# Performance work log

Measured on AMD Instinct MI355X. Metric: run time of the kernel, lower is better.

## Reference

```python
import jax, jax.numpy as jnp
import numpy as np

N_GRID, N_IO = 99872, 128   # height*width, n_inputs+n_outputs
N = N_GRID + N_IO           # 100000 nodes
E = 1600000                 # edges before self-loops
HID, WID = 128, 128         # hidden_dim, network_width (heads=1)


def _ln(h, g, b, eps=1e-5):
    mu = jnp.mean(h, axis=-1, keepdims=True)
    v = jnp.mean((h - mu) ** 2, axis=-1, keepdims=True)
    return (h - mu) * jax.lax.rsqrt(v + eps) * g + b


def setup_inputs() -> dict:
    ks = jax.random.split(jax.random.key(0), 32)
    r = lambda i, sh, s=0.05: jax.random.normal(ks[i], sh, jnp.float32) * s
    return {
        "x": jax.random.normal(ks[0], (N, HID + 2), jnp.float32),
        "edge_index": jax.random.randint(ks[1], (2, E), 0, N),
        "initial": r(2, (N_IO, HID)),
        "Wf1": r(3, (HID + 2, WID)), "bf1": r(4, (WID,)),
        "Wf2": r(5, (WID, HID + 2)), "bf2": r(6, (HID + 2,)),
        "Wu1": r(7, (HID + 2, WID)), "bu1": r(8, (WID,)),
        "Wu2": r(9, (WID, HID)), "bu2": r(10, (HID,)),
        "Wc1": r(11, (HID + 2, WID)), "bc1": r(12, (WID,)),
        "Wc2": r(13, (WID, WID)), "bc2": r(14, (WID,)),
        "Wc3": r(15, (WID, WID)), "bc3": r(16, (WID,)),
        "Wc4": r(17, (WID, WID)), "bc4": r(18, (WID,)),
        "Wco": r(19, (WID, HID)), "bco": r(20, (HID,)),
        "g3": jnp.ones((WID,), jnp.float32), "bn3": jnp.zeros((WID,), jnp.float32),
        "g6": jnp.ones((WID,), jnp.float32), "bn6": jnp.zeros((WID,), jnp.float32),
        "g7": jnp.ones((WID,), jnp.float32), "bn7": jnp.zeros((WID,), jnp.float32),
    }


def _step(x, initial, Wf1, bf1, Wf2, bf2, Wu1, bu1, Wu2, bu2,
          Wc1, bc1, Wc2, bc2, Wc3, bc3, Wc4, bc4, Wco, bco,
          g3, bn3, g6, bn6, g7, bn7, edge_index):
    # GCNConv: add self-loops, symmetric deg^-1/2 normalization, max-aggregation.
    loops = jnp.arange(N)
    row = jnp.concatenate([edge_index[0], loops])  # source
    col = jnp.concatenate([edge_index[1], loops])  # target
    deg = jax.ops.segment_sum(jnp.ones(row.shape[0], x.dtype), col, num_segments=N)
    dinv = jnp.where(deg > 0, jax.lax.rsqrt(deg), 0.0)
    norm = dinv[row] * dinv[col]  # [E+N]

    def gcn(h, W, b):
        m = (h @ W)[row] * norm[:, None]                      # gather + scale
        return jax.ops.segment_max(m, col, num_segments=N) + b  # scatter-max

    # forget gate, mixing toward the (padded) initial state
    f = jax.nn.sigmoid(jax.nn.sigmoid(x @ Wf1 + bf1) @ Wf2 + bf2)  # [N, HID+2]
    init_pad = jnp.concatenate([jnp.zeros((N_GRID, HID), x.dtype), initial], axis=0)
    init_pad = jnp.concatenate([init_pad, jnp.zeros((N, 2), x.dtype)], axis=1)
    x = x * f + (1.0 - f) * init_pad

    # update gate
    u = jax.nn.sigmoid(jax.nn.sigmoid(x @ Wu1 + bu1) @ Wu2 + bu2)  # [N, HID]

    h = jax.nn.relu(_ln(gcn(x, Wc1, bc1), g3, bn3))
    h = _ln(gcn(h, Wc2, bc2), g3, bn3)   # layer_norm3 reused, as in source
    h = _ln(gcn(h, Wc3, bc3), g6, bn6)
    h = _ln(gcn(h, Wc4, bc4), g7, bn7)
    h = gcn(h, Wco, bco)                 # [N, HID]
    return x[:, :-2] + h * u


def reference(x, edge_index, initial, Wf1, bf1, Wf2, bf2, Wu1, bu1, Wu2, bu2,
              Wc1, bc1, Wc2, bc2, Wc3, bc3, Wc4, bc4, Wco, bco,
              g3, bn3, g6, bn6, g7, bn7):
    return _step(x, initial, Wf1, bf1, Wf2, bf2, Wu1, bu1, Wu2, bu2,
                 Wc1, bc1, Wc2, bc2, Wc3, bc3, Wc4, bc4, Wco, bco,
                 g3, bn3, g6, bn6, g7, bn7, edge_index)
```

## Files before the change

kernel.cpp:

```cpp
#include <hip/hip_runtime.h>
#include <cstdint>

#define HID 128
#define HC  130
#define NIO 128
#define DENSW 64
#define SUBB 8
#define BCAP_S 128

typedef _Float16 f16;
typedef _Float16 f16x2 __attribute__((ext_vector_type(2)));
typedef _Float16 f16x4 __attribute__((ext_vector_type(4)));
typedef _Float16 f16x8 __attribute__((ext_vector_type(8)));
typedef float    f32x4 __attribute__((ext_vector_type(4)));

__device__ __forceinline__ float sigm(float z) {
  return 1.0f / (1.0f + __expf(-z));
}

__device__ __forceinline__ int xcc_id() {
  int x;
  asm volatile("s_getreg_b32 %0, hwreg(HW_REG_XCC_ID)" : "=s"(x));
  return x & 7;
}

__device__ __forceinline__ f16x8 max8(f16x8 a, f16x8 b) {
  union P { f16x8 h; f16x2 p[4]; } A, B, O;
  A.h = a; B.h = b;
  #pragma unroll
  for (int i = 0; i < 4; ++i)
    asm("v_pk_max_f16 %0, %1, %2" : "=v"(O.p[i]) : "v"(A.p[i]), "v"(B.p[i]));
  return O.h;
}

struct WDesc { const float* src; f16* dst; int K, NC, Kpad, NCpad; };
struct WAll { WDesc m[9]; };

__global__ __launch_bounds__(256) void prep_kernel(
    const float* __restrict__ x, f16* __restrict__ x16, f16* __restrict__ xg,
    int n, WAll wa, int* __restrict__ bcnt, int nzero, int gX) {
  const int bb = blockIdx.x;
  const int t = threadIdx.x;
  if (bb < gX) {
    int idx = bb * 256 + t;
    if (idx >= n * 20) return;
    int r = idx / 20, g = idx - r * 20;
    int c0 = g * 8;
    f16x8 o;
    #pragma unroll
    for (int j = 0; j < 8; ++j) {
      int c = c0 + j;
      o[j] = (f16)((c < HC) ? x[(size_t)r * HC + c] : 0.0f);
    }
    *(f16x8*)&x16[(size_t)r * 160 + c0] = o;
    if (c0 >= 136) {
      f16x8 z = (f16x8){0,0,0,0,0,0,0,0};
      *(f16x8*)&xg[(size_t)r * 160 + c0] = z;
    } else if (c0 == 128) {
      #pragma unroll
      for (int c = 130; c < 136; ++c) xg[(size_t)r * 160 + c] = (f16)0.0f;
    }
  } else if (bb < gX + 90) {
    const int wb = bb - gX;
    const WDesc d = wa.m[wb / 10];
    const int KST = d.Kpad >> 5;
    const int total = (d.NCpad >> 4) * KST * 64;
    int idx = (wb % 10) * 256 + t;
    if (idx >= total) return;
    int nt  = idx / (KST * 64);
    int rem = idx - nt * (KST * 64);
    int ks  = rem >> 6;
    int l   = rem & 63;
    int nn  = nt * 16 + (l & 15);
    int k0  = ks * 32 + (l >> 4) * 8;
    f16x8 o;
    #pragma unroll
    for (int j = 0; j < 8; ++j) {
      int k = k0 + j;
      float v = (k < d.K && nn < d.NC) ? d.src[(size_t)k * d.NC + nn] : 0.0f;
      o[j] = (f16)v;
    }
    *((f16x8*)d.dst + idx) = o;
  } else {
    int i = (bb - gX - 90) * 256 + t;
    if (i < nzero) bcnt[i] = 0;
  }
}

__global__ void binscatter_kernel(const int* __restrict__ row, const int* __restrict__ col,
    int* __restrict__ bcnt, unsigned* __restrict__ bucket, int e, int nb) {
  const int g0 = xcc_id() * SUBB + ((blockIdx.x >> 3) & (SUBB - 1));
  int i = blockIdx.x * blockDim.x + threadIdx.x;
  if (i >= e) return;
  int c = col[i], r = row[i];
  int b = c >> 7;
  int cur = atomicAdd(&bcnt[g0 * nb + b], 1);
  if (cur < BCAP_S)
    bucket[((size_t)g0 * nb + b) * BCAP_S + cur] = ((unsigned)r << 7) | (unsigned)(c & 127);
}

__global__ __launch_bounds__(256) void build_kernel(const int* __restrict__ bcnt,
    const unsigned* __restrict__ bucket, int* __restrict__ ncnt,
    int* __restrict__ dense, float* __restrict__ dinv, int n, int nb) {
  __shared__ int lcnt[128];
  const int b = blockIdx.x;
  const int t = threadIdx.x;
  if (t < 128) lcnt[t] = 0;
  __syncthreads();
  const int wv = t >> 6, ln = t & 63;
  #pragma unroll 1
  for (int g = wv * 16; g < wv * 16 + 16; ++g) {
    const int cntg = min(bcnt[g * nb + b], BCAP_S);
    const unsigned* __restrict__ src = bucket + ((size_t)g * nb + b) * BCAP_S;
    for (int idx = ln; idx < cntg; idx += 64) {
      unsigned ev = src[idx];
      int cl = (int)(ev & 127u);
      int r  = (int)(ev >> 7);
      int s = atomicAdd(&lcnt[cl], 1);
      if (s < DENSW) dense[(size_t)((b << 7) + cl) * DENSW + s] = r;
    }
  }
  __syncthreads();
  if (t < 128) {
    int c = (b << 7) + t;
    if (c < n) {
      int cc = min(lcnt[t], DENSW);
      ncnt[c] = cc;
      dinv[c] = rsqrtf((float)(cc + 1));
    }
  }
}

template<int KPAD, int RS, int NCPAD, int NC, int MODE, int MROWS>
__global__ __launch_bounds__(256, 4) void mm_mfma(
    const f16* __restrict__ X, const f16* __restrict__ Wt,
    const float* __restrict__ bias, f16* __restrict__ Y,
    const float* __restrict__ dinv, const f16* __restrict__ xor16,
    const float* __restrict__ initial, int n, int ngrid)
{
  static_assert(MODE != 1 || MROWS == 128, "MODE1 only at 128 rows");
  constexpr int KST = KPAD / 32;
  constexpr int NT  = NCPAD / 16;
  constexpr int MT  = MROWS / 64;
  constexpr int RPW = MROWS / 4;
  constexpr int YRS = (MODE == 1) ? 160 : 128;
  constexpr int PSTR = (NCPAD == 128) ? 132 : 148;
  constexpr int LDSH = (NCPAD * KPAD > MROWS * PSTR) ? NCPAD * KPAD : MROWS * PSTR;
  __shared__ __align__(16) f16 Bs[LDSH];

  const int t = threadIdx.x;
  const int wid  = t >> 6;
  const int l    = t & 63;
  const int m15  = l & 15;
  const int quad = l >> 4;
  const int rw   = blockIdx.x * MROWS + wid * RPW;

  constexpr int BSW = NCPAD * KPAD / 8;
  #pragma unroll
  for (int i = 0; i < (BSW + 255) / 256; ++i) {
    int idx = t + i * 256;
    if (BSW % 256 == 0 || idx < BSW)
      ((f16x8*)Bs)[idx] = ((const f16x8*)Wt)[idx];
  }

  const f16* Xr0 = X + (size_t)(rw + m15) * RS;
  const f16* Xr1 = X + (size_t)(rw + 16 + m15) * RS;
  f16x8 a0r[KST], a1r[KST];
  #pragma unroll
  for (int ks = 0; ks < KST; ++ks) {
    const int off = ks * 32 + quad * 8;
    a0r[ks] = *(const f16x8*)(Xr0 + off);
    if constexpr (MT == 2) a1r[ks] = *(const f16x8*)(Xr1 + off);
  }

  constexpr int TPR = 256 / MROWS;
  constexpr int CSP = 128 / TPR;
  const int r  = t / TPR;
  const int cp = t % TPR;
  const int gr = blockIdx.x * MROWS + r;
  float dv = 0.0f;
  if constexpr (MODE == 2) dv = (gr < n) ? dinv[gr] : 0.0f;

  f16x8 xo[CSP / 8];
  f16x2 xo2;
  if constexpr (MODE == 1) {
    const f16* xp = xor16 + (size_t)gr * 160;
    #pragma unroll
    for (int c8 = 0; c8 < CSP / 8; ++c8)
      xo[c8] = *(const f16x8*)(xp + cp * CSP + c8 * 8);
    xo2 = *(const f16x2*)(xp + 128);
  }

  __syncthreads();

  f32x4 acc[MT][NT];
  #pragma unroll
  for (int mt = 0; mt < MT; ++mt)
    #pragma unroll
    for (int nt = 0; nt < NT; ++nt)
      acc[mt][nt] = (f32x4){0.f, 0.f, 0.f, 0.f};

  #pragma unroll
  for (int ks = 0; ks < KST; ++ks) {
    #pragma unroll
    for (int nt = 0; nt < NT; ++nt) {
      f16x8 b = *((const f16x8*)Bs + (nt * KST + ks) * 64 + l);
      acc[0][nt] = __builtin_amdgcn_mfma_f32_16x16x32_f16(a0r[ks], b, acc[0][nt], 0, 0, 0);
      if constexpr (MT == 2)
        acc[1][nt] = __builtin_amdgcn_mfma_f32_16x16x32_f16(a1r[ks], b, acc[1][nt], 0, 0, 0);
    }
  }

  __syncthreads();

  #pragma unroll
  for (int mt = 0; mt < MT; ++mt) {
    #pragma unroll
    for (int reg = 0; reg < 4; ++reg) {
      const int rl = wid * RPW + mt * 16 + quad * 4 + reg;
      #pragma unroll
      for (int nt = 0; nt < NT; ++nt)
        Bs[rl * PSTR + nt * 16 + m15] = (f16)acc[mt][nt][reg];
    }
  }
  __syncthreads();

  if (gr < n) {
    if constexpr (MODE == 0 || MODE == 2) {
      #pragma unroll
      for (int c8 = 0; c8 < CSP / 8; ++c8) {
        const int c0 = cp * CSP + c8 * 8;
        f16x8 v = *(const f16x8*)&Bs[r * PSTR + c0];
        f16x8 o;
        #pragma unroll
        for (int j = 0; j < 8; ++j) {
          float a = (float)v[j];
          if constexpr (MODE == 0) o[j] = (f16)sigm(a + bias[c0 + j]);
          else                     o[j] = (f16)(a * dv);
        }
        *(f16x8*)&Y[(size_t)gr * YRS + c0] = o;
      }
    } else {
      const bool hasInit = (gr >= ngrid);
      #pragma unroll
      for (int c8 = 0; c8 < CSP / 8; ++c8) {
        const int c0 = cp * CSP + c8 * 8;
        f16x8 v = *(const f16x8*)&Bs[r * PSTR + c0];
        f16x8 o;
        #pragma unroll
        for (int j = 0; j < 8; ++j) {
          const int col = c0 + j;
          float fv = sigm((float)v[j] + bias[col]);
          float xov = (float)xo[c8][j];
          float ip = hasInit ? initial[(size_t)(gr - ngrid) * 128 + col] : 0.0f;
          o[j] = (f16)(xov * fv + (1.0f - fv) * ip);
        }
        *(f16x8*)&Y[(size_t)gr * YRS + c0] = o;
      }
      if (cp == 1) {
        #pragma unroll
        for (int k = 0; k < 2; ++k) {
          const int col = 128 + k;
          float fv = sigm((float)Bs[r * PSTR + col] + bias[col]);
          Y[(size_t)gr * YRS + col] = (f16)((float)xo2[k] * fv);
        }
      }
    }
  }
}

template<int K1PAD, int RS1, int NC2PAD, int NC2, int MODE2>
__global__ __launch_bounds__(256, 2) void mm_fused(
    const f16* __restrict__ X, const f16* __restrict__ W1t, const f16* __restrict__ W2t,
    const float* __restrict__ b1, const float* __restrict__ b2, f16* __restrict__ Y,
    const f16* __restrict__ xor16, const float* __restrict__ initial, int n, int ngrid)
{
  constexpr int KST1 = K1PAD / 32;
  constexpr int NT1  = 8;
  constexpr int KST2 = 4;
  constexpr int NT2  = NC2PAD / 16;
  constexpr int PSTR1 = 132;
  constexpr int PSTR2 = (NC2PAD == 128) ? 132 : 148;
  constexpr int YRS  = (MODE2 == 1) ? 160 : 128;
  constexpr int W2U  = NC2PAD * 128;
  constexpr int SC_A = K1PAD * 128;
  constexpr int SC_B = 128 * PSTR2;
  constexpr int SCU  = (SC_A > SC_B) ? SC_A : SC_B;
  __shared__ __align__(16) f16 L[W2U + SCU];
  f16* Bs2 = L;
  f16* SC  = L + W2U;

  const int t = threadIdx.x;
  const int wid  = t >> 6;
  const int l    = t & 63;
  const int m15  = l & 15;
  const int quad = l >> 4;
  const int rw   = blockIdx.x * 128 + wid * 32;

  constexpr int W1W = K1PAD * 128 / 8;
  constexpr int W2W = NC2PAD * 128 / 8;
  for (int i = t; i < W1W; i += 256) ((f16x8*)SC)[i]  = ((const f16x8*)W1t)[i];
  for (int i = t; i < W2W; i += 256) ((f16x8*)Bs2)[i] = ((const f16x8*)W2t)[i];

  const f16* Xr0 = X + (size_t)(rw + m15) * RS1;
  const f16* Xr1 = X + (size_t)(rw + 16 + m15) * RS1;
  f16x8 a0r[KST1], a1r[KST1];
  #pragma unroll
  for (int ks = 0; ks < KST1; ++ks) {
    const int off = ks * 32 + quad * 8;
    a0r[ks] = *(const f16x8*)(Xr0 + off);
    a1r[ks] = *(const f16x8*)(Xr1 + off);
  }

  f16x8 xo[8];
  f16x2 xo2;
  if constexpr (MODE2 == 1) {
    const f16* xp = xor16 + (size_t)(blockIdx.x * 128 + (t >> 1)) * 160;
    #pragma unroll
    for (int c8 = 0; c8 < 8; ++c8)
      xo[c8] = *(const f16x8*)(xp + (t & 1) * 64 + c8 * 8);
    xo2 = *(const f16x2*)(xp + 128);
  }

  float b1r[NT1];
  #pragma unroll
  for (int nt = 0; nt < NT1; ++nt) b1r[nt] = b1[nt * 16 + m15];

  __syncthreads();

  f32x4 acc1[2][NT1];
  #pragma unroll
  for (int mt = 0; mt < 2; ++mt)
    #pragma unroll
    for (int nt = 0; nt < NT1; ++nt)
      acc1[mt][nt] = (f32x4){0.f, 0.f, 0.f, 0.f};

  #pragma unroll
  for (int ks = 0; ks < KST1; ++ks) {
    #pragma unroll
    for (int nt = 0; nt < NT1; ++nt) {
      f16x8 b = *((const f16x8*)SC + (nt * KST1 + ks) * 64 + l);
      acc1[0][nt] = __builtin_amdgcn_mfma_f32_16x16x32_f16(a0r[ks], b, acc1[0][nt], 0, 0, 0);
      acc1[1][nt] = __builtin_amdgcn_mfma_f32_16x16x32_f16(a1r[ks], b, acc1[1][nt], 0, 0, 0);
    }
  }

  __syncthreads();

  #pragma unroll
  for (int mt = 0; mt < 2; ++mt) {
    #pragma unroll
    for (int reg = 0; reg < 4; ++reg) {
      const int rl = wid * 32 + mt * 16 + quad * 4 + reg;
      #pragma unroll
      for (int nt = 0; nt < NT1; ++nt)
        SC[rl * PSTR1 + nt * 16 + m15] = (f16)sigm(acc1[mt][nt][reg] + b1r[nt]);
    }
  }
  __syncthreads();

  f32x4 acc2[2][NT2];
  #pragma unroll
  for (int mt = 0; mt < 2; ++mt)
    #pragma unroll
    for (int nt = 0; nt < NT2; ++nt)
      acc2[mt][nt] = (f32x4){0.f, 0.f, 0.f, 0.f};

  const int rA0 = wid * 32 + m15;
  const int rA1 = rA0 + 16;
  union A8 { f16x8 v; f16x4 q[2]; };
  #pragma unroll
  for (int ks = 0; ks < KST2; ++ks) {
    const int k0 = ks * 32 + quad * 8;
    A8 a0, a1;
    a0.q[0] = *(const f16x4*)&SC[rA0 * PSTR1 + k0];
    a0.q[1] = *(const f16x4*)&SC[rA0 * PSTR1 + k0 + 4];
    a1.q[0] = *(const f16x4*)&SC[rA1 * PSTR1 + k0];
    a1.q[1] = *(const f16x4*)&SC[rA1 * PSTR1 + k0 + 4];
    #pragma unroll
    for (int nt = 0; nt < NT2; ++nt) {
      f16x8 b = *((const f16x8*)Bs2 + (nt * KST2 + ks) * 64 + l);
      acc2[0][nt] = __builtin_amdgcn_mfma_f32_16x16x32_f16(a0.v, b, acc2[0][nt], 0, 0, 0);
      acc2[1][nt] = __builtin_amdgcn_mfma_f32_16x16x32_f16(a1.v, b, acc2[1][nt], 0, 0, 0);
    }
  }
  __syncthreads();

  #pragma unroll
  for (int mt = 0; mt < 2; ++mt) {
    #pragma unroll
    for (int reg = 0; reg < 4; ++reg) {
      const int rl = wid * 32 + mt * 16 + quad * 4 + reg;
      #pragma unroll
      for (int nt = 0; nt < NT2; ++nt)
        SC[rl * PSTR2 + nt * 16 + m15] = (f16)acc2[mt][nt][reg];
    }
  }
  __syncthreads();

  const int r  = t >> 1;
  const int hf = t & 1;
  const int gr = blockIdx.x * 128 + r;
  if (gr < n) {
    if constexpr (MODE2 == 0) {
      #pragma unroll
      for (int c8 = 0; c8 < 8; ++c8) {
        const int c0 = hf * 64 + c8 * 8;
        f16x8 v = *(const f16x8*)&SC[r * PSTR2 + c0];
        f16x8 o;
        #pragma unroll
        for (int j = 0; j < 8; ++j)
          o[j] = (f16)sigm((float)v[j] + b2[c0 + j]);
        *(f16x8*)&Y[(size_t)gr * YRS + c0] = o;
      }
    } else {
      const bool hasInit = (gr >= ngrid);
      #pragma unroll
      for (int c8 = 0; c8 < 8; ++c8) {
        const int c0 = hf * 64 + c8 * 8;
        f16x8 v = *(const f16x8*)&SC[r * PSTR2 + c0];
        f16x8 o;
        #pragma unroll
        for (int j = 0; j < 8; ++j) {
          const int col = c0 + j;
          float fv = sigm((float)v[j] + b2[col]);
          float xov = (float)xo[c8][j];
          float ip = hasInit ? initial[(size_t)(gr - ngrid) * 128 + col] : 0.0f;
          o[j] = (f16)(xov * fv + (1.0f - fv) * ip);
        }
        *(f16x8*)&Y[(size_t)gr * YRS + c0] = o;
      }
      if (hf) {
        #pragma unroll
        for (int k = 0; k < 2; ++k) {
          const int col = 128 + k;
          float fv = sigm((float)SC[r * PSTR2 + col] + b2[col]);
          Y[(size_t)gr * YRS + col] = (f16)((float)xo2[k] * fv);
        }
      }
    }
  }
}

template<int MODE>
__global__ __launch_bounds__(256) void agg_kernel(
    const f16* __restrict__ G, const int* __restrict__ ncnt,
    const int* __restrict__ dense,
    const float* __restrict__ dinv, const float* __restrict__ bias,
    const float* __restrict__ gamma, const float* __restrict__ beta,
    const f16* __restrict__ xg, const f16* __restrict__ u,
    void* __restrict__ out, int n)
{
  const int wid = threadIdx.x >> 6, lane = threadIdx.x & 63;
  const int c = blockIdx.x * 4 + wid;
  if (c >= n) return;
  const int li = lane & 15, grp = lane >> 4;

  union F8 { f16x8 h; int4 i; };
  const int nc = min(ncnt[c], DENSW);
  int raw = 0;
  if (lane < 32) raw = dense[(size_t)c * DENSW + lane];
  if (nc > 32) {
    if (lane >= 32) raw = dense[(size_t)c * DENSW + lane];
  }
  const int myidx = (lane < nc) ? raw : c;

  F8 m; m.h = *(const f16x8*)(G + (size_t)c * 128 + li * 8);
  F8 m2; m2.h = m.h;
  F8 m3; m3.h = m.h;
  F8 m4; m4.h = m.h;
  const int B = (nc + 3) >> 2;
  int b = 0;
  for (; b + 3 < B; b += 4) {
    int r0 = __shfl(myidx, (b + 0) * 4 + grp, 64);
    int r1 = __shfl(myidx, (b + 1) * 4 + grp, 64);
    int r2 = __shfl(myidx, (b + 2) * 4 + grp, 64);
    int r3 = __shfl(myidx, (b + 3) * 4 + grp, 64);
    F8 v0; v0.h = *(const f16x8*)(G + (size_t)r0 * 128 + li * 8);
    F8 v1; v1.h = *(const f16x8*)(G + (size_t)r1 * 128 + li * 8);
    F8 v2; v2.h = *(const f16x8*)(G + (size_t)r2 * 128 + li * 8);
    F8 v3; v3.h = *(const f16x8*)(G + (size_t)r3 * 128 + li * 8);
    m.h  = max8(m.h,  v0.h);
    m2.h = max8(m2.h, v1.h);
    m3.h = max8(m3.h, v2.h);
    m4.h = max8(m4.h, v3.h);
  }
  for (; b < B; ++b) {
    int r0 = __shfl(myidx, b * 4 + grp, 64);
    F8 v; v.h = *(const f16x8*)(G + (size_t)r0 * 128 + li * 8);
    m.h = max8(m.h, v.h);
  }
  m.h = max8(max8(m.h, m2.h), max8(m3.h, m4.h));

  #pragma unroll
  for (int st = 16; st <= 32; st <<= 1) {
    F8 o;
    #pragma unroll
    for (int d = 0; d < 4; ++d) o.i[d] = __shfl_xor(m.i[d], st, 64);
    m.h = max8(m.h, o.h);
  }

  const float dc = dinv[c];
  float v[8];
  float s = 0.f, sq = 0.f;
  #pragma unroll
  for (int j = 0; j < 8; ++j) {
    v[j] = (float)m.h[j] * dc + bias[li * 8 + j];
    s += v[j]; sq += v[j] * v[j];
  }

  if constexpr (MODE == 2) {
    if (grp == 0) {
      f16x8 xv = *(const f16x8*)(xg + (size_t)c * 160 + li * 8);
      f16x8 uv = *(const f16x8*)(u  + (size_t)c * 128 + li * 8);
      float o[8];
      #pragma unroll
      for (int j = 0; j < 8; ++j) o[j] = (float)xv[j] + v[j] * (float)uv[j];
      float* op = (float*)out + (size_t)c * 128 + li * 8;
      *(float4*)op       = make_float4(o[0], o[1], o[2], o[3]);
      *(float4*)(op + 4) = make_float4(o[4], o[5], o[6], o[7]);
    }
  } else {
    #pragma unroll
    for (int st = 1; st <= 8; st <<= 1) {
      s  += __shfl_xor(s, st, 64);
      sq += __shfl_xor(sq, st, 64);
    }
    float mu  = s * (1.0f / 128.0f);
    float var = sq * (1.0f / 128.0f) - mu * mu;
    float rstd = rsqrtf(var + 1e-5f);
    if (grp == 0) {
      f16x8 ov;
      #pragma unroll
      for (int j = 0; j < 8; ++j) {
        float o = (v[j] - mu) * rstd * gamma[li * 8 + j] + beta[li * 8 + j];
        if constexpr (MODE == 0) o = fmaxf(o, 0.0f);
        ov[j] = (f16)o;
      }
      *(f16x8*)((f16*)out + (size_t)c * 128 + li * 8) = ov;
    }
  }
}

extern "C" void kernel_launch(void* const* d_in, const int* in_sizes, int n_in,
                              void* d_out, int out_size, void* d_ws, size_t ws_size,
                              hipStream_t stream) {
  (void)n_in; (void)out_size; (void)ws_size;
  const float* x       = (const float*)d_in[0];
  const int*   ei      = (const int*)d_in[1];
  const float* initial = (const float*)d_in[2];
  const float* Wf1 = (const float*)d_in[3];  const float* bf1 = (const float*)d_in[4];
  const float* Wf2 = (const float*)d_in[5];  const float* bf2 = (const float*)d_in[6];
  const float* Wu1 = (const float*)d_in[7];  const float* bu1 = (const float*)d_in[8];
  const float* Wu2 = (const float*)d_in[9];  const float* bu2 = (const float*)d_in[10];
  const float* Wc1 = (const float*)d_in[11]; const float* bc1 = (const float*)d_in[12];
  const float* Wc2 = (const float*)d_in[13]; const float* bc2 = (const float*)d_in[14];
  const float* Wc3 = (const float*)d_in[15]; const float* bc3 = (const float*)d_in[16];
  const float* Wc4 = (const float*)d_in[17]; const float* bc4 = (const float*)d_in[18];
  const float* Wco = (const float*)d_in[19]; const float* bco = (const float*)d_in[20];
  const float* g3  = (const float*)d_in[21]; const float* bn3 = (const float*)d_in[22];
  const float* g6  = (const float*)d_in[23]; const float* bn6 = (const float*)d_in[24];
  const float* g7  = (const float*)d_in[25]; const float* bn7 = (const float*)d_in[26];

  const int N  = in_sizes[0] / HC;
  const int E  = in_sizes[1] / 2;
  const int NG = N - NIO;
  const int NP = N + 128;
  const int NB = (N + 127) / 128;
  const int NSEG = 8 * SUBB;

  char* w = (char*)d_ws;
  auto carve = [&](size_t bytes) {
    char* p = w; w += (bytes + 255) & ~(size_t)255; return p;
  };
  int*      bcnt   = (int*)     carve((size_t)NB * NSEG * 4);
  unsigned* bucket = (unsigned*)carve((size_t)NB * NSEG * BCAP_S * 4);
  int*      ncnt   = (int*)     carve((size_t)N * 4);
  int*      dense  = (int*)     carve((size_t)N * DENSW * 4);
  float*    dinv   = (float*)   carve((size_t)N * 4);
  f16*      x16    = (f16*)     carve((size_t)NP * 160 * 2);
  f16*      xg     = (f16*)     carve((size_t)NP * 160 * 2);
  f16*      u      = (f16*)     carve((size_t)N  * 128 * 2);
  f16*      G      = (f16*)     carve((size_t)N  * 128 * 2);
  f16*      H      = (f16*)     carve((size_t)NP * 128 * 2);
  f16*      Wt_f1  = (f16*)     carve(160 * 128 * 2);
  f16*      Wt_f2  = (f16*)     carve(128 * 144 * 2);
  f16*      Wt_u1  = (f16*)     carve(160 * 128 * 2);
  f16*      Wt_u2  = (f16*)     carve(128 * 128 * 2);
  f16*      Wt_c1  = (f16*)     carve(160 * 128 * 2);
  f16*      Wt_c2  = (f16*)     carve(128 * 128 * 2);
  f16*      Wt_c3  = (f16*)     carve(128 * 128 * 2);
  f16*      Wt_c4  = (f16*)     carve(128 * 128 * 2);
  f16*      Wt_co  = (f16*)     carve(128 * 128 * 2);

  const int* erow = ei;
  const int* ecol = ei + E;

  const int gE  = (E + 255) / 256;
  const int gM  = (N + 127) / 128;
  const int gM64 = (N + 63) / 64;
  const int gA  = (N + 3) / 4;

  WAll wa;
  wa.m[0] = {Wf1, Wt_f1, HC,  HID, 160, 128};
  wa.m[1] = {Wf2, Wt_f2, HID, HC,  128, 144};
  wa.m[2] = {Wu1, Wt_u1, HC,  HID, 160, 128};
  wa.m[3] = {Wu2, Wt_u2, HID, HID, 128, 128};
  wa.m[4] = {Wc1, Wt_c1, HC,  HID, 160, 128};
  wa.m[5] = {Wc2, Wt_c2, HID, HID, 128, 128};
  wa.m[6] = {Wc3, Wt_c3, HID, HID, 128, 128};
  wa.m[7] = {Wc4, Wt_c4, HID, HID, 128, 128};
  wa.m[8] = {Wco, Wt_co, HID, HID, 128, 128};
  const int gX = (N * 20 + 255) / 256;
  const int gZ = (NB * NSEG + 255) / 256;
  prep_kernel<<<gX + 90 + gZ, 256, 0, stream>>>(x, x16, xg, N, wa, bcnt, NB * NSEG, gX);

  binscatter_kernel<<<gE, 256, 0, stream>>>(erow, ecol, bcnt, bucket, E, NB);
  build_kernel<<<NB, 256, 0, stream>>>(bcnt, bucket, ncnt, dense, dinv, N, NB);

  mm_fused<160, 160, 144, 130, 1><<<gM, 256, 0, stream>>>(
      x16, Wt_f1, Wt_f2, bf1, bf2, xg, x16, initial, N, NG);
  mm_fused<160, 160, 128, 128, 0><<<gM, 256, 0, stream>>>(
      xg, Wt_u1, Wt_u2, bu1, bu2, u, nullptr, nullptr, N, NG);

  mm_mfma<160, 160, 128, 128, 2, 64><<<gM64, 256, 0, stream>>>(xg, Wt_c1, nullptr, G, dinv, nullptr, nullptr, N, NG);
  agg_kernel<0><<<gA, 256, 0, stream>>>(G, ncnt, dense, dinv, bc1, g3, bn3, nullptr, nullptr, H, N);
  mm_mfma<128, 128, 128, 128, 2, 64><<<gM64, 256, 0, stream>>>(H, Wt_c2, nullptr, G, dinv, nullptr, nullptr, N, NG);
  agg_kernel<1><<<gA, 256, 0, stream>>>(G, ncnt, dense, dinv, bc2, g3, bn3, nullptr, nullptr, H, N);
  mm_mfma<128, 128, 128, 128, 2, 64><<<gM64, 256, 0, stream>>>(H, Wt_c3, nullptr, G, dinv, nullptr, nullptr, N, NG);
  agg_kernel<1><<<gA, 256, 0, stream>>>(G, ncnt, dense, dinv, bc3, g6, bn6, nullptr, nullptr, H, N);
  mm_mfma<128, 128, 128, 128, 2, 64><<<gM64, 256, 0, stream>>>(H, Wt_c4, nullptr, G, dinv, nullptr, nullptr, N, NG);
  agg_kernel<1><<<gA, 256, 0, stream>>>(G, ncnt, dense, dinv, bc4, g7, bn7, nullptr, nullptr, H, N);
  mm_mfma<128, 128, 128, 128, 2, 64><<<gM64, 256, 0, stream>>>(H, Wt_co, nullptr, G, dinv, nullptr, nullptr, N, NG);
  agg_kernel<2><<<gA, 256, 0, stream>>>(G, ncnt, dense, dinv, bco, nullptr, nullptr, xg, u, d_out, N);
}
```

Before: 725.9 us.

## Fuse max-aggregation and LayerNorm with next layer's GEMM into one kernel

Replaces the separate agg_kernel and mm_mfma launches for GCN layers 2-5 with a single aggmm_kernel. Each block aggregates 64 nodes into a shared-memory tile, applies LayerNorm, runs the next 128x128 MFMA matmul from that tile and writes the dinv-scaled result to a ping-pong G buffer. This removes four launches and the global write and re-read of the intermediate H activations. In exchange, each wave walks 16 nodes serially before the matmul, which may cut memory-level parallelism during the gather. The B fragments are read straight from global memory instead of staged in LDS, and the unused MODE 1 path in mm_mfma is deleted.

After: 802.5 us. 10.6% more time.

```diff
diff --git a/kernel.cpp b/kernel.cpp
--- a/kernel.cpp
+++ b/kernel.cpp
@@ -181,16 +181,6 @@
   float dv = 0.0f;
   if constexpr (MODE == 2) dv = (gr < n) ? dinv[gr] : 0.0f;
 
-  f16x8 xo[CSP / 8];
-  f16x2 xo2;
-  if constexpr (MODE == 1) {
-    const f16* xp = xor16 + (size_t)gr * 160;
-    #pragma unroll
-    for (int c8 = 0; c8 < CSP / 8; ++c8)
-      xo[c8] = *(const f16x8*)(xp + cp * CSP + c8 * 8);
-    xo2 = *(const f16x2*)(xp + 128);
-  }
-
   __syncthreads();
 
   f32x4 acc[MT][NT];
@@ -226,45 +216,18 @@
   __syncthreads();
 
   if (gr < n) {
-    if constexpr (MODE == 0 || MODE == 2) {
-      #pragma unroll
-      for (int c8 = 0; c8 < CSP / 8; ++c8) {
-        const int c0 = cp * CSP + c8 * 8;
-        f16x8 v = *(const f16x8*)&Bs[r * PSTR + c0];
-        f16x8 o;
-        #pragma unroll
-        for (int j = 0; j < 8; ++j) {
-          float a = (float)v[j];
-          if constexpr (MODE == 0) o[j] = (f16)sigm(a + bias[c0 + j]);
-          else                     o[j] = (f16)(a * dv);
-        }
-        *(f16x8*)&Y[(size_t)gr * YRS + c0] = o;
-      }
-    } else {
-      const bool hasInit = (gr >= ngrid);
-      #pragma unroll
-      for (int c8 = 0; c8 < CSP / 8; ++c8) {
-        const int c0 = cp * CSP + c8 * 8;
-        f16x8 v = *(const f16x8*)&Bs[r * PSTR + c0];
-        f16x8 o;
-        #pragma unroll
-        for (int j = 0; j < 8; ++j) {
-          const int col = c0 + j;
-          float fv = sigm((float)v[j] + bias[col]);
-          float xov = (float)xo[c8][j];
-          float ip = hasInit ? initial[(size_t)(gr - ngrid) * 128 + col] : 0.0f;
-          o[j] = (f16)(xov * fv + (1.0f - fv) * ip);
-        }
-        *(f16x8*)&Y[(size_t)gr * YRS + c0] = o;
-      }
-      if (cp == 1) {
-        #pragma unroll
-        for (int k = 0; k < 2; ++k) {
-          const int col = 128 + k;
-          float fv = sigm((float)Bs[r * PSTR + col] + bias[col]);
-          Y[(size_t)gr * YRS + col] = (f16)((float)xo2[k] * fv);
-        }
-      }
+    #pragma unroll
+    for (int c8 = 0; c8 < CSP / 8; ++c8) {
+      const int c0 = cp * CSP + c8 * 8;
+      f16x8 v = *(const f16x8*)&Bs[r * PSTR + c0];
+      f16x8 o;
+      #pragma unroll
+      for (int j = 0; j < 8; ++j) {
+        float a = (float)v[j];
+        if constexpr (MODE == 0) o[j] = (f16)sigm(a + bias[c0 + j]);
+        else                     o[j] = (f16)(a * dv);
+      }
+      *(f16x8*)&Y[(size_t)gr * YRS + c0] = o;
     }
   }
 }
@@ -442,14 +405,152 @@
   }
 }
 
-template<int MODE>
-__global__ __launch_bounds__(256) void agg_kernel(
+template<int LNMODE>
+__global__ __launch_bounds__(256, 5) void aggmm_kernel(
     const f16* __restrict__ G, const int* __restrict__ ncnt,
-    const int* __restrict__ dense,
-    const float* __restrict__ dinv, const float* __restrict__ bias,
-    const float* __restrict__ gamma, const float* __restrict__ beta,
-    const f16* __restrict__ xg, const f16* __restrict__ u,
-    void* __restrict__ out, int n)
+    const int* __restrict__ dense, const float* __restrict__ dinv,
+    const float* __restrict__ bias, const float* __restrict__ gamma,
+    const float* __restrict__ beta, const f16* __restrict__ Wt,
+    f16* __restrict__ Gout, int n)
+{
+  constexpr int PSTR = 132;
+  __shared__ __align__(16) f16 Htile[64 * PSTR];
+
+  const int t = threadIdx.x;
+  const int wv = t >> 6, lane = t & 63;
+  const int li = lane & 15, grp = lane >> 4;
+  const int cbase = blockIdx.x * 64;
+
+  union F8 { f16x8 h; int4 i; };
+
+  #pragma unroll 1
+  for (int i = 0; i < 16; ++i) {
+    const int lr = wv * 16 + i;
+    const int c = cbase + lr;
+    if (c < n) {
+      const int nc = min(ncnt[c], DENSW);
+      int raw = 0;
+      if (lane < 32) raw = dense[(size_t)c * DENSW + lane];
+      if (nc > 32) {
+        if (lane >= 32) raw = dense[(size_t)c * DENSW + lane];
+      }
+      const int myidx = (lane < nc) ? raw : c;
+
+      F8 m; m.h = *(const f16x8*)(G + (size_t)c * 128 + li * 8);
+      F8 m2; m2.h = m.h;
+      F8 m3; m3.h = m.h;
+      F8 m4; m4.h = m.h;
+      const int B = (nc + 3) >> 2;
+      int b = 0;
+      for (; b + 3 < B; b += 4) {
+        int r0 = __shfl(myidx, (b + 0) * 4 + grp, 64);
+        int r1 = __shfl(myidx, (b + 1) * 4 + grp, 64);
+        int r2 = __shfl(myidx, (b + 2) * 4 + grp, 64);
+        int r3 = __shfl(myidx, (b + 3) * 4 + grp, 64);
+        F8 v0; v0.h = *(const f16x8*)(G + (size_t)r0 * 128 + li * 8);
+        F8 v1; v1.h = *(const f16x8*)(G + (size_t)r1 * 128 + li * 8);
+        F8 v2; v2.h = *(const f16x8*)(G + (size_t)r2 * 128 + li * 8);
+        F8 v3; v3.h = *(const f16x8*)(G + (size_t)r3 * 128 + li * 8);
+        m.h  = max8(m.h,  v0.h);
+        m2.h = max8(m2.h, v1.h);
+        m3.h = max8(m3.h, v2.h);
+        m4.h = max8(m4.h, v3.h);
+      }
+      for (; b < B; ++b) {
+        int r0 = __shfl(myidx, b * 4 + grp, 64);
+        F8 v; v.h = *(const f16x8*)(G + (size_t)r0 * 128 + li * 8);
+        m.h = max8(m.h, v.h);
+      }
+      m.h = max8(max8(m.h, m2.h), max8(m3.h, m4.h));
+
+      #pragma unroll
+      for (int st = 16; st <= 32; st <<= 1) {
+        F8 o;
+        #pragma unroll
+        for (int d = 0; d < 4; ++d) o.i[d] = __shfl_xor(m.i[d], st, 64);
+        m.h = max8(m.h, o.h);
+      }
+
+      const float dc = dinv[c];
+      float v[8];
+      float s = 0.f, sq = 0.f;
+      #pragma unroll
+      for (int j = 0; j < 8; ++j) {
+        v[j] = (float)m.h[j] * dc + bias[li * 8 + j];
+        s += v[j]; sq += v[j] * v[j];
+      }
+      #pragma unroll
+      for (int st = 1; st <= 8; st <<= 1) {
+        s  += __shfl_xor(s, st, 64);
+        sq += __shfl_xor(sq, st, 64);
+      }
+      float mu  = s * (1.0f / 128.0f);
+      float var = sq * (1.0f / 128.0f) - mu * mu;
+      float rstd = rsqrtf(var + 1e-5f);
+      if (grp == 0) {
+        f16x8 ov;
+        #pragma unroll
+        for (int j = 0; j < 8; ++j) {
+          float o = (v[j] - mu) * rstd * gamma[li * 8 + j] + beta[li * 8 + j];
+          if constexpr (LNMODE == 0) o = fmaxf(o, 0.0f);
+          ov[j] = (f16)o;
+        }
+        *(f16x8*)&Htile[lr * PSTR + li * 8] = ov;
+      }
+    }
+  }
+  __syncthreads();
+
+  const int m15 = lane & 15, quad = lane >> 4;
+  f16x8 a[4];
+  #pragma unroll
+  for (int ks = 0; ks < 4; ++ks)
+    a[ks] = *(const f16x8*)&Htile[(wv * 16 + m15) * PSTR + ks * 32 + quad * 8];
+
+  f32x4 acc[8];
+  #pragma unroll
+  for (int nt = 0; nt < 8; ++nt) acc[nt] = (f32x4){0.f, 0.f, 0.f, 0.f};
+  #pragma unroll
+  for (int ks = 0; ks < 4; ++ks) {
+    #pragma unroll
+    for (int nt = 0; nt < 8; ++nt) {
+      f16x8 b = *((const f16x8*)Wt + (nt * 4 + ks) * 64 + lane);
+      acc[nt] = __builtin_amdgcn_mfma_f32_16x16x32_f16(a[ks], b, acc[nt], 0, 0, 0);
+    }
+  }
+  __syncthreads();
+
+  #pragma unroll
+  for (int reg = 0; reg < 4; ++reg) {
+    const int rl = wv * 16 + quad * 4 + reg;
+    #pragma unroll
+    for (int nt = 0; nt < 8; ++nt)
+      Htile[rl * PSTR + nt * 16 + m15] = (f16)acc[nt][reg];
+  }
+  __syncthreads();
+
+  const int r  = t >> 2;
+  const int cp = t & 3;
+  const int gr = cbase + r;
+  if (gr < n) {
+    const float dv = dinv[gr];
+    #pragma unroll
+    for (int c8 = 0; c8 < 4; ++c8) {
+      const int c0 = cp * 32 + c8 * 8;
+      f16x8 v = *(const f16x8*)&Htile[r * PSTR + c0];
+      f16x8 o;
+      #pragma unroll
+      for (int j = 0; j < 8; ++j) o[j] = (f16)((float)v[j] * dv);
+      *(f16x8*)&Gout[(size_t)gr * 128 + c0] = o;
+    }
+  }
+}
+
+__global__ __launch_bounds__(256) void aggfin_kernel(
+    const f16* __restrict__ G, const int* __restrict__ ncnt,
+    const int* __restrict__ dense, const float* __restrict__ dinv,
+    const float* __restrict__ bias, const f16* __restrict__ xg,
+    const f16* __restrict__ u, float* __restrict__ out, int n)
 {
   const int wid = threadIdx.x >> 6, lane = threadIdx.x & 63;
   const int c = blockIdx.x * 4 + wid;
@@ -500,45 +601,19 @@
     m.h = max8(m.h, o.h);
   }
 
-  const float dc = dinv[c];
-  float v[8];
-  float s = 0.f, sq = 0.f;
-  #pragma unroll
-  for (int j = 0; j < 8; ++j) {
-    v[j] = (float)m.h[j] * dc + bias[li * 8 + j];
-    s += v[j]; sq += v[j] * v[j];
-  }
-
-  if constexpr (MODE == 2) {
-    if (grp == 0) {
-      f16x8 xv = *(const f16x8*)(xg + (size_t)c * 160 + li * 8);
-      f16x8 uv = *(const f16x8*)(u  + (size_t)c * 128 + li * 8);
-      float o[8];
-      #pragma unroll
-      for (int j = 0; j < 8; ++j) o[j] = (float)xv[j] + v[j] * (float)uv[j];
-      float* op = (float*)out + (size_t)c * 128 + li * 8;
-      *(float4*)op       = make_float4(o[0], o[1], o[2], o[3]);
-      *(float4*)(op + 4) = make_float4(o[4], o[5], o[6], o[7]);
-    }
-  } else {
-    #pragma unroll
-    for (int st = 1; st <= 8; st <<= 1) {
-      s  += __shfl_xor(s, st, 64);
-      sq += __shfl_xor(sq, st, 64);
-    }
-    float mu  = s * (1.0f / 128.0f);
-    float var = sq * (1.0f / 128.0f) - mu * mu;
-    float rstd = rsqrtf(var + 1e-5f);
-    if (grp == 0) {
-      f16x8 ov;
-      #pragma unroll
-      for (int j = 0; j < 8; ++j) {
-        float o = (v[j] - mu) * rstd * gamma[li * 8 + j] + beta[li * 8 + j];
-        if constexpr (MODE == 0) o = fmaxf(o, 0.0f);
-        ov[j] = (f16)o;
-      }
-      *(f16x8*)((f16*)out + (size_t)c * 128 + li * 8) = ov;
-    }
+  if (grp == 0) {
+    const float dc = dinv[c];
+    f16x8 xv = *(const f16x8*)(xg + (size_t)c * 160 + li * 8);
+    f16x8 uv = *(const f16x8*)(u  + (size_t)c * 128 + li * 8);
+    float o[8];
+    #pragma unroll
+    for (int j = 0; j < 8; ++j) {
+      float v = (float)m.h[j] * dc + bias[li * 8 + j];
+      o[j] = (float)xv[j] + v * (float)uv[j];
+    }
+    float* op = out + (size_t)c * 128 + li * 8;
+    *(float4*)op       = make_float4(o[0], o[1], o[2], o[3]);
+    *(float4*)(op + 4) = make_float4(o[4], o[5], o[6], o[7]);
   }
 }
 
@@ -581,8 +656,8 @@
   f16*      x16    = (f16*)     carve((size_t)NP * 160 * 2);
   f16*      xg     = (f16*)     carve((size_t)NP * 160 * 2);
   f16*      u      = (f16*)     carve((size_t)N  * 128 * 2);
-  f16*      G      = (f16*)     carve((size_t)N  * 128 * 2);
-  f16*      H      = (f16*)     carve((size_t)NP * 128 * 2);
+  f16*      G      = (f16*)     carve((size_t)NP * 128 * 2);
+  f16*      G2     = (f16*)     carve((size_t)NP * 128 * 2);
   f16*      Wt_f1  = (f16*)     carve(160 * 128 * 2);
   f16*      Wt_f2  = (f16*)     carve(128 * 144 * 2);
   f16*      Wt_u1  = (f16*)     carve(160 * 128 * 2);
@@ -596,10 +671,11 @@
   const int* erow = ei;
   const int* ecol = ei + E;
 
-  const int gE  = (E + 255) / 256;
-  const int gM  = (N + 127) / 128;
+  const int gE   = (E + 255) / 256;
+  const int gM   = (N + 127) / 128;
   const int gM64 = (N + 63) / 64;
-  const int gA  = (N + 3) / 4;
+  const int gA   = (N + 3) / 4;
+  const int gAM  = (N + 63) / 64;
 
   WAll wa;
   wa.m[0] = {Wf1, Wt_f1, HC,  HID, 160, 128};
@@ -623,14 +699,11 @@
   mm_fused<160, 160, 128, 128, 0><<<gM, 256, 0, stream>>>(
       xg, Wt_u1, Wt_u2, bu1, bu2, u, nullptr, nullptr, N, NG);
 
-  mm_mfma<160, 160, 128, 128, 2, 64><<<gM64, 256, 0, stream>>>(xg, Wt_c1, nullptr, G, dinv, nullptr, nullptr, N, NG);
-  agg_kernel<0><<<gA, 256, 0, stream>>>(G, ncnt, dense, dinv, bc1, g3, bn3, nullptr, nullptr, H, N);
-  mm_mfma<128, 128, 128, 128, 2, 64><<<gM64, 256, 0, stream>>>(H, Wt_c2, nullptr, G, dinv, nullptr, nullptr, N, NG);
-  agg_kernel<1><<<gA, 256, 0, stream>>>(G, ncnt, dense, dinv, bc2, g3, bn3, nullptr, nullptr, H, N);
-  mm_mfma<128, 128, 128, 128, 2, 64><<<gM64, 256, 0, stream>>>(H, Wt_c3, nullptr, G, dinv, nullptr, nullptr, N, NG);
-  agg_kernel<1><<<gA, 256, 0, stream>>>(G, ncnt, dense, dinv, bc3, g6, bn6, nullptr, nullptr, H, N);
-  mm_mfma<128, 128, 128, 128, 2, 64><<<gM64, 256, 0, stream>>>(H, Wt_c4, nullptr, G, dinv, nullptr, nullptr, N, NG);
-  agg_kernel<1><<<gA, 256, 0, stream>>>(G, ncnt, dense, dinv, bc4, g7, bn7, nullptr, nullptr, H, N);
-  mm_mfma<128, 128, 128, 128, 2, 64><<<gM64, 256, 0, stream>>>(H, Wt_co, nullptr, G, dinv, nullptr, nullptr, N, NG);
-  agg_kernel<2><<<gA, 256, 0, stream>>>(G, ncnt, dense, dinv, bco, nullptr, nullptr, xg, u, d_out, N);
-}
+  mm_mfma<160, 160, 128, 128, 2, 64><<<gM64, 256, 0, stream>>>(
+      xg, Wt_c1, nullptr, G, dinv, nullptr, nullptr, N, NG);
+  aggmm_kernel<0><<<gAM, 256, 0, stream>>>(G,  ncnt, dense, dinv, bc1, g3, bn3, Wt_c2, G2, N);
+  aggmm_kernel<1><<<gAM, 256, 0, stream>>>(G2, ncnt, dense, dinv, bc2, g3, bn3, Wt_c3, G,  N);
+  aggmm_kernel<1><<<gAM, 256, 0, stream>>>(G,  ncnt, dense, dinv, bc3, g6, bn6, Wt_c4, G2, N);
+  aggmm_kernel<1><<<gAM, 256, 0, stream>>>(G2, ncnt, dense, dinv, bc4, g7, bn7, Wt_co, G,  N);
+  aggfin_kernel<<<gA, 256, 0, stream>>>(G, ncnt, dense, dinv, bco, xg, u, (float*)d_out, N);
+}
```
